# Performance work log

Hardware: AMD Instinct MI355X
Metric: run time of the kernel (lower is better)

Reference implementation:

```python
import jax, jax.numpy as jnp
import numpy as np

B, DIM, HID, K, G, MID = 1024, 384, 64, 8, 48, 128
EPS = 1e-06


def _gaussian_8x8():
    t = jnp.arange(K, dtype=jnp.float32) - 3.5
    g = jnp.exp(-(t[:, None] ** 2 + t[None, :] ** 2) / (2.0 * 2.0 ** 2))
    return g / g.sum()


def setup_inputs() -> dict:
    key = jax.random.key(0)
    ks = jax.random.split(key, 16)
    inp = {
        "x": jax.random.normal(ks[0], (B, DIM), dtype=jnp.float32),
        "W": jax.random.normal(ks[1], (DIM, HID), dtype=jnp.float32) * 0.02,
        "b": jax.random.normal(ks[2], (DIM, HID), dtype=jnp.float32) * 0.02,
        "patch_weight": _gaussian_8x8(),  # learnable 8x8, softmaxed in forward
        "pair_w1": jax.random.normal(ks[3], (G, G), dtype=jnp.float32) * 0.02,
        "pair_b1": jax.random.normal(ks[4], (G, G), dtype=jnp.float32) * 0.02,
        "pair_w2": jax.random.normal(ks[5], (G, G), dtype=jnp.float32) * 0.02,
        "pair_b2": jax.random.normal(ks[6], (G, G), dtype=jnp.float32) * 0.02,
        # nn.Linear(G, DIM)
        "proj_w": jax.random.normal(ks[7], (DIM, G), dtype=jnp.float32) * (1.0 / np.sqrt(G)),
        "proj_b": jax.random.normal(ks[8], (DIM,), dtype=jnp.float32) * 0.02,
        # nn.Linear(HID, MID)
        "down_w": jax.random.normal(ks[9], (MID, HID), dtype=jnp.float32) * (1.0 / np.sqrt(HID)),
        "down_b": jax.random.normal(ks[10], (MID,), dtype=jnp.float32) * 0.02,
        # nn.Linear(MID, HID)
        "up_w": jax.random.normal(ks[11], (HID, MID), dtype=jnp.float32) * (1.0 / np.sqrt(MID)),
        "up_b": jax.random.normal(ks[12], (HID,), dtype=jnp.float32) * 0.02,
    }
    return inp


def _leaky(v):
    return jnp.where(v >= 0, v, 0.01 * v)


def reference(x, W, b, patch_weight, pair_w1, pair_b1, pair_w2, pair_b2,
              proj_w, proj_b, down_w, down_b, up_w, up_b):
    # scale / inverse-bias GELU features: (B, DIM, HID)
    s = x[:, :, None]
    inv = 1.0 / (jnp.abs(s) + EPS)
    H = jax.nn.gelu(s * W[None] + inv * b[None], approximate=False)
    # Gram matrix over hidden dim: (B, DIM, DIM)
    P = jnp.einsum('bik,bjk->bij', H, H)
    # learnable gaussian patch pooling (softmax over flattened 8x8 weights)
    w = jax.nn.softmax(patch_weight.reshape(-1)).reshape(K, K)
    Pg = jnp.einsum('bgkhl,kl->bgh', P.reshape(-1, G, K, G, K), w)  # (B, G, G)
    # two elementwise gated leaky layers
    Pg = _leaky(Pg * pair_w1[None] + pair_b1[None])
    Pg = _leaky(Pg * pair_w2[None] + pair_b2[None])
    # softmax + nonlinear row reduction -> (B, G)
    row_soft = jax.nn.softmax(Pg, axis=-1)
    row_weights = (1.0 / (1.0 + row_soft ** 2)).sum(axis=-1)
    # project 48 -> 384, scale rows of H
    scales = row_weights @ proj_w.T + proj_b  # (B, DIM)
    H = H * scales[:, :, None]
    # tiny MLP on hidden dim
    z = _leaky(H @ down_w.T + down_b)
    z = _leaky(z @ up_w.T + up_b)
    return z
```

## Files before the change

kernel.cpp:

```cpp
#include <hip/hip_runtime.h>


#define EPSF 1e-6f

typedef __attribute__((ext_vector_type(8))) short bf16x8;
typedef __attribute__((ext_vector_type(4))) float f32x4;
typedef __attribute__((ext_vector_type(4))) unsigned short u16x4;

__device__ __forceinline__ unsigned short f2bf(float f) {
    union { float f; unsigned int u; } v; v.f = f;
    unsigned int r = v.u + 0x7fffu + ((v.u >> 16) & 1u);
    return (unsigned short)(r >> 16);
}
__device__ __forceinline__ float bf2f(unsigned short h) {
    union { unsigned int u; float f; } v; v.u = ((unsigned int)h) << 16;
    return v.f;
}
__device__ __forceinline__ float leaky(float v) { return fmaxf(v, 0.01f * v); }
__device__ __forceinline__ int key8(int r) { return (r ^ (r >> 3)) & 7; }
__device__ __forceinline__ float gelu_f(float u) {
    float t = u * (1.5957691216f + 0.0713548163f * (u * u));
    float e = __expf(t);
    float r = __builtin_amdgcn_rcpf(e + 1.0f);
    return fmaf(-u, r, u);
}

__global__ void prep(const float* __restrict__ proj_w,
                     const float* __restrict__ down_w,
                     const float* __restrict__ up_w,
                     float* __restrict__ ws) {
    int idx = blockIdx.x * blockDim.x + threadIdx.x;
    unsigned short* wb = (unsigned short*)(ws + 18432);
    if (idx < 18432) {
        int i = idx / 48, g = idx % 48;
        ws[g * 384 + i] = proj_w[idx];
    } else if (idx < 26624) {
        int k = idx - 18432;
        wb[k] = f2bf(down_w[k]);
    } else if (idx < 34816) {
        int k = idx - 26624;
        wb[8192 + k] = f2bf(up_w[k]);
    }
}

__global__ __launch_bounds__(1024, 4) void fused_main(
    const float* __restrict__ x,
    const float* __restrict__ W,
    const float* __restrict__ bb,
    const float* __restrict__ patch_weight,
    const float* __restrict__ pw1, const float* __restrict__ pb1,
    const float* __restrict__ pw2, const float* __restrict__ pb2,
    const float* __restrict__ proj_b,
    const float* __restrict__ down_b,
    const float* __restrict__ up_b,
    const float* __restrict__ ws,
    float* __restrict__ out)
{
    __shared__ __align__(16) unsigned short sH[24576];
    __shared__ __align__(16) unsigned short sRB[24576];
    __shared__ __align__(16) unsigned short sZ1[24576];
    __shared__ float sw[64];
    __shared__ float srw[48];
    __shared__ float sScale[384];
    __shared__ float sDb[128];
    __shared__ float sUb[64];

    const int t = threadIdx.x;
    const int b = blockIdx.x;
    const int wv = t >> 6, lane = t & 63, q = lane >> 4, r = lane & 15;
    const float* projT = ws;
    const unsigned short* dwB = (const unsigned short*)(ws + 18432);
    const unsigned short* uwB = dwB + 8192;
    unsigned short* sM  = sRB;
    unsigned short* sDW = sRB;
    unsigned short* sUW = sRB + 8192;
    float* sPg = (float*)(sRB + 16384);

    if (t < 64) {
        float p = patch_weight[t];
        float m = p;
        for (int o = 32; o > 0; o >>= 1) m = fmaxf(m, __shfl_xor(m, o));
        float e = __expf(p - m);
        float s = e;
        for (int o = 32; o > 0; o >>= 1) s += __shfl_xor(s, o);
        sw[t] = e * __builtin_amdgcn_rcpf(s);
    }

    for (int j = 0; j < 6; ++j) {
        int idx4 = j * 1024 + t;
        int base = idx4 * 4;
        int i = base >> 6, c0 = base & 63;
        float4 w4 = ((const float4*)W)[idx4];
        float4 b4 = ((const float4*)bb)[idx4];
        float xi  = x[b * 384 + i];
        float inv = __builtin_amdgcn_rcpf(fabsf(xi) + EPSF);
        u16x4 hv;
        hv[0] = f2bf(gelu_f(fmaf(xi, w4.x, inv * b4.x)));
        hv[1] = f2bf(gelu_f(fmaf(xi, w4.y, inv * b4.y)));
        hv[2] = f2bf(gelu_f(fmaf(xi, w4.z, inv * b4.z)));
        hv[3] = f2bf(gelu_f(fmaf(xi, w4.w, inv * b4.w)));
        int cb = c0 >> 3, cc = c0 & 7;
        *(u16x4*)&sH[i * 64 + ((cb ^ key8(i)) << 3) + cc] = hv;
    }
    __syncthreads();

    if (t < 768) {
        const int cb = t & 7, lq = (t >> 3) & 1, g = t >> 4;
        float acc[4][8];
        #pragma unroll
        for (int a = 0; a < 4; ++a)
            #pragma unroll
            for (int cc = 0; cc < 8; ++cc) acc[a][cc] = 0.0f;
        #pragma unroll
        for (int k = 0; k < 8; ++k) {
            int i = g * 8 + k;
            bf16x8 hv = *(const bf16x8*)&sH[i * 64 + ((cb ^ key8(i)) << 3)];
            f32x4 w4 = *(const f32x4*)&sw[k * 8 + lq * 4];
            float hf[8];
            #pragma unroll
            for (int cc = 0; cc < 8; ++cc) hf[cc] = bf2f((unsigned short)hv[cc]);
            #pragma unroll
            for (int a = 0; a < 4; ++a)
                #pragma unroll
                for (int cc = 0; cc < 8; ++cc) acc[a][cc] = fmaf(w4[a], hf[cc], acc[a][cc]);
        }
        #pragma unroll
        for (int a = 0; a < 4; ++a) {
            int l = lq * 4 + a;
            bf16x8 mv;
            #pragma unroll
            for (int cc = 0; cc < 8; ++cc) mv[cc] = (short)f2bf(acc[a][cc]);
            *(bf16x8*)&sM[g * 512 + ((l * 8 + (cb ^ key8(g))) << 3)] = mv;
        }
    }
    __syncthreads();

    f32x4 pacc = {0.f, 0.f, 0.f, 0.f};
    if (wv < 9) {
        const int tg = wv / 3, th = wv % 3;
        for (int ks = 0; ks < 16; ++ks) {
            int kf = ks * 32 + q * 8;
            int g = tg * 16 + r;
            int cbg = kf >> 3;
            int cbs = (cbg & ~7) | ((cbg ^ key8(g)) & 7);
            bf16x8 av = *(const bf16x8*)&sM[g * 512 + (cbs << 3)];
            int h = th * 16 + r;
            int i = h * 8 + (kf >> 6);
            int cbh = (kf & 63) >> 3;
            bf16x8 bv = *(const bf16x8*)&sH[i * 64 + ((cbh ^ key8(i)) << 3)];
            pacc = __builtin_amdgcn_mfma_f32_16x16x32_bf16(av, bv, pacc, 0, 0, 0);
        }
        #pragma unroll
        for (int reg = 0; reg < 4; ++reg) {
            int g = tg * 16 + q * 4 + reg;
            int h = th * 16 + r;
            int idx = g * 48 + h;
            float v = pacc[reg];
            v = leaky(fmaf(v, pw1[idx], pb1[idx]));
            v = leaky(fmaf(v, pw2[idx], pb2[idx]));
            pacc[reg] = v;
        }
    }
    __syncthreads();

    if (wv < 9) {
        const int tg = wv / 3, th = wv % 3;
        #pragma unroll
        for (int reg = 0; reg < 4; ++reg) {
            int g = tg * 16 + q * 4 + reg;
            int h = th * 16 + r;
            sPg[g * 49 + h] = pacc[reg];
        }
    } else {
        for (int cid = t - 576; cid < 2048; cid += 448) {
            if (cid < 1024) {
                int nrow = cid >> 3, cb = cid & 7;
                bf16x8 v = *(const bf16x8*)&dwB[cid * 8];
                *(bf16x8*)&sDW[nrow * 64 + ((cb ^ key8(nrow)) << 3)] = v;
            } else {
                int c2 = cid - 1024;
                int rrow = c2 >> 4, cb = c2 & 15;
                bf16x8 v = *(const bf16x8*)&uwB[c2 * 8];
                int cbs = (cb & 8) | ((cb ^ key8(rrow)) & 7);
                *(bf16x8*)&sUW[rrow * 128 + (cbs << 3)] = v;
            }
        }
    }
    if (t < 128) sDb[t] = down_b[t];
    else if (t < 192) sUb[t - 128] = up_b[t - 128];
    __syncthreads();

    {
        #pragma unroll
        for (int rr = 0; rr < 3; ++rr) {
            int row = wv + rr * 16;
            float v = (lane < 48) ? sPg[row * 49 + lane] : -1e30f;
            float m = v;
            for (int o = 32; o > 0; o >>= 1) m = fmaxf(m, __shfl_xor(m, o));
            float e = (lane < 48) ? __expf(v - m) : 0.0f;
            float s = e;
            for (int o = 32; o > 0; o >>= 1) s += __shfl_xor(s, o);
            float p = e * __builtin_amdgcn_rcpf(s);
            float rwv = (lane < 48) ? __builtin_amdgcn_rcpf(fmaf(p, p, 1.0f)) : 0.0f;
            for (int o = 32; o > 0; o >>= 1) rwv += __shfl_xor(rwv, o);
            if (lane == 0) srw[row] = rwv;
        }
    }
    __syncthreads();

    if (t < 384) {
        float s = proj_b[t];
        #pragma unroll 4
        for (int g = 0; g < 48; ++g) s = fmaf(srw[g], projT[g * 384 + t], s);
        sScale[t] = s;
    }
    __syncthreads();

    const int mg = wv >> 2, ng = wv & 3;
    for (int rt = 0; rt < 2; ++rt) {
        const int r0 = rt * 192;
        {
            f32x4 zacc[3][2];
            #pragma unroll
            for (int a = 0; a < 3; ++a)
                #pragma unroll
                for (int e = 0; e < 2; ++e) zacc[a][e] = (f32x4){0.f, 0.f, 0.f, 0.f};
            #pragma unroll
            for (int ks = 0; ks < 2; ++ks) {
                int cb = ks * 4 + q;
                bf16x8 af[3];
                #pragma unroll
                for (int a = 0; a < 3; ++a) {
                    int i = r0 + (mg * 3 + a) * 16 + r;
                    af[a] = *(const bf16x8*)&sH[i * 64 + ((cb ^ key8(i)) << 3)];
                }
                #pragma unroll
                for (int e = 0; e < 2; ++e) {
                    int n = (ng * 2 + e) * 16 + r;
                    bf16x8 bv = *(const bf16x8*)&sDW[n * 64 + ((cb ^ key8(n)) << 3)];
                    #pragma unroll
                    for (int a = 0; a < 3; ++a)
                        zacc[a][e] = __builtin_amdgcn_mfma_f32_16x16x32_bf16(af[a], bv, zacc[a][e], 0, 0, 0);
                }
            }
            #pragma unroll
            for (int a = 0; a < 3; ++a) {
                #pragma unroll
                for (int e = 0; e < 2; ++e) {
                    #pragma unroll
                    for (int reg = 0; reg < 4; ++reg) {
                        int rl = (mg * 3 + a) * 16 + q * 4 + reg;
                        int m = (ng * 2 + e) * 16 + r;
                        float v = leaky(fmaf(zacc[a][e][reg], sScale[r0 + rl], sDb[m]));
                        int cb2 = m >> 3;
                        int cbs2 = (cb2 & 8) | ((cb2 ^ key8(rl)) & 7);
                        sZ1[rl * 128 + (cbs2 << 3) + (m & 7)] = f2bf(v);
                    }
                }
            }
        }
        __syncthreads();
        {
            f32x4 oacc[3];
            #pragma unroll
            for (int a = 0; a < 3; ++a) oacc[a] = (f32x4){0.f, 0.f, 0.f, 0.f};
            #pragma unroll
            for (int ks = 0; ks < 4; ++ks) {
                int cb = ks * 4 + q;
                int cp = ng * 16 + r;
                int cbsB = (cb & 8) | ((cb ^ key8(cp)) & 7);
                bf16x8 bv = *(const bf16x8*)&sUW[cp * 128 + (cbsB << 3)];
                #pragma unroll
                for (int a = 0; a < 3; ++a) {
                    int rl = (mg * 3 + a) * 16 + r;
                    int cbsA = (cb & 8) | ((cb ^ key8(rl)) & 7);
                    bf16x8 av = *(const bf16x8*)&sZ1[rl * 128 + (cbsA << 3)];
                    oacc[a] = __builtin_amdgcn_mfma_f32_16x16x32_bf16(av, bv, oacc[a], 0, 0, 0);
                }
            }
            #pragma unroll
            for (int a = 0; a < 3; ++a) {
                #pragma unroll
                for (int reg = 0; reg < 4; ++reg) {
                    int i = r0 + (mg * 3 + a) * 16 + q * 4 + reg;
                    int cp = ng * 16 + r;
                    out[(b * 384 + i) * 64 + cp] = leaky(oacc[a][reg] + sUb[cp]);
                }
            }
        }
        __syncthreads();
    }
}

extern "C" void kernel_launch(void* const* d_in, const int* in_sizes, int n_in,
                              void* d_out, int out_size, void* d_ws, size_t ws_size,
                              hipStream_t stream) {
    const float* x      = (const float*)d_in[0];
    const float* W      = (const float*)d_in[1];
    const float* bb     = (const float*)d_in[2];
    const float* pw     = (const float*)d_in[3];
    const float* pw1    = (const float*)d_in[4];
    const float* pb1    = (const float*)d_in[5];
    const float* pw2    = (const float*)d_in[6];
    const float* pb2    = (const float*)d_in[7];
    const float* proj_w = (const float*)d_in[8];
    const float* proj_b = (const float*)d_in[9];
    const float* down_w = (const float*)d_in[10];
    const float* down_b = (const float*)d_in[11];
    const float* up_w   = (const float*)d_in[12];
    const float* up_b   = (const float*)d_in[13];
    float* out = (float*)d_out;
    float* ws  = (float*)d_ws;

    prep<<<(34816 + 255) / 256, 256, 0, stream>>>(proj_w, down_w, up_w, ws);
    fused_main<<<1024, 1024, 0, stream>>>(x, W, bb, pw, pw1, pb1, pw2, pb2,
                                          proj_b, down_b, up_b, ws, out);
}
```

Measured before the change: 197.6 us.

## Split fused kernel into scale kernel and MLP kernel with recomputed GELU

The single 1024-thread fused kernel becomes two kernels. The first computes H, the pooled Gram matrix and the per-row scales with 512 threads, doing the pooling and MFMA work in two rounds to halve the sM buffer, then writes the scales to workspace. The second runs 3072 smaller blocks that recompute H in registers for 128 rows each and apply the down/up MLP. This lowers shared memory per block and should raise occupancy and parallelism, at the cost of recomputing the GELU features, an extra launch and a global round trip for the scales.

```diff
diff --git a/kernel.cpp b/kernel.cpp
--- a/kernel.cpp
+++ b/kernel.cpp
@@ -21,9 +21,11 @@
 __device__ __forceinline__ float gelu_f(float u) {
     float t = u * (1.5957691216f + 0.0713548163f * (u * u));
     float e = __expf(t);
-    float r = __builtin_amdgcn_rcpf(e + 1.0f);
-    return fmaf(-u, r, u);
-}
+    float rc = __builtin_amdgcn_rcpf(e + 1.0f);
+    return fmaf(-u, rc, u);
+}
+
+#define SCALES_OFF 26624
 
 __global__ void prep(const float* __restrict__ proj_w,
                      const float* __restrict__ down_w,
@@ -43,7 +45,7 @@
     }
 }
 
-__global__ __launch_bounds__(1024, 4) void fused_main(
+__global__ __launch_bounds__(512, 4) void kernA(
     const float* __restrict__ x,
     const float* __restrict__ W,
     const float* __restrict__ bb,
@@ -51,30 +53,18 @@
     const float* __restrict__ pw1, const float* __restrict__ pb1,
     const float* __restrict__ pw2, const float* __restrict__ pb2,
     const float* __restrict__ proj_b,
-    const float* __restrict__ down_b,
-    const float* __restrict__ up_b,
     const float* __restrict__ ws,
-    float* __restrict__ out)
+    float* __restrict__ scales)
 {
     __shared__ __align__(16) unsigned short sH[24576];
-    __shared__ __align__(16) unsigned short sRB[24576];
-    __shared__ __align__(16) unsigned short sZ1[24576];
-    __shared__ float sw[64];
+    __shared__ __align__(16) unsigned short sM[12288];
+    __shared__ __align__(16) float sw[64];
     __shared__ float srw[48];
-    __shared__ float sScale[384];
-    __shared__ float sDb[128];
-    __shared__ float sUb[64];
-
-    const int t = threadIdx.x;
-    const int b = blockIdx.x;
+    float* sPg = (float*)sM;
+
+    const int t = threadIdx.x, b = blockIdx.x;
     const int wv = t >> 6, lane = t & 63, q = lane >> 4, r = lane & 15;
     const float* projT = ws;
-    const unsigned short* dwB = (const unsigned short*)(ws + 18432);
-    const unsigned short* uwB = dwB + 8192;
-    unsigned short* sM  = sRB;
-    unsigned short* sDW = sRB;
-    unsigned short* sUW = sRB + 8192;
-    float* sPg = (float*)(sRB + 16384);
 
     if (t < 64) {
         float p = patch_weight[t];
@@ -86,8 +76,8 @@
         sw[t] = e * __builtin_amdgcn_rcpf(s);
     }
 
-    for (int j = 0; j < 6; ++j) {
-        int idx4 = j * 1024 + t;
+    for (int j = 0; j < 12; ++j) {
+        int idx4 = j * 512 + t;
         int base = idx4 * 4;
         int i = base >> 6, c0 = base & 63;
         float4 w4 = ((const float4*)W)[idx4];
@@ -104,107 +94,92 @@
     }
     __syncthreads();
 
-    if (t < 768) {
-        const int cb = t & 7, lq = (t >> 3) & 1, g = t >> 4;
-        float acc[4][8];
-        #pragma unroll
-        for (int a = 0; a < 4; ++a)
-            #pragma unroll
-            for (int cc = 0; cc < 8; ++cc) acc[a][cc] = 0.0f;
-        #pragma unroll
-        for (int k = 0; k < 8; ++k) {
-            int i = g * 8 + k;
-            bf16x8 hv = *(const bf16x8*)&sH[i * 64 + ((cb ^ key8(i)) << 3)];
-            f32x4 w4 = *(const f32x4*)&sw[k * 8 + lq * 4];
-            float hf[8];
-            #pragma unroll
-            for (int cc = 0; cc < 8; ++cc) hf[cc] = bf2f((unsigned short)hv[cc]);
+    f32x4 pacc[2];
+    pacc[0] = (f32x4){0.f, 0.f, 0.f, 0.f};
+    pacc[1] = (f32x4){0.f, 0.f, 0.f, 0.f};
+    for (int rnd = 0; rnd < 2; ++rnd) {
+        if (t < 384) {
+            const int g = t >> 3, cb = t & 7;
+            float acc[4][8];
             #pragma unroll
             for (int a = 0; a < 4; ++a)
                 #pragma unroll
-                for (int cc = 0; cc < 8; ++cc) acc[a][cc] = fmaf(w4[a], hf[cc], acc[a][cc]);
-        }
-        #pragma unroll
-        for (int a = 0; a < 4; ++a) {
-            int l = lq * 4 + a;
-            bf16x8 mv;
+                for (int cc = 0; cc < 8; ++cc) acc[a][cc] = 0.0f;
             #pragma unroll
-            for (int cc = 0; cc < 8; ++cc) mv[cc] = (short)f2bf(acc[a][cc]);
-            *(bf16x8*)&sM[g * 512 + ((l * 8 + (cb ^ key8(g))) << 3)] = mv;
-        }
-    }
-    __syncthreads();
-
-    f32x4 pacc = {0.f, 0.f, 0.f, 0.f};
-    if (wv < 9) {
-        const int tg = wv / 3, th = wv % 3;
-        for (int ks = 0; ks < 16; ++ks) {
-            int kf = ks * 32 + q * 8;
-            int g = tg * 16 + r;
-            int cbg = kf >> 3;
-            int cbs = (cbg & ~7) | ((cbg ^ key8(g)) & 7);
-            bf16x8 av = *(const bf16x8*)&sM[g * 512 + (cbs << 3)];
-            int h = th * 16 + r;
-            int i = h * 8 + (kf >> 6);
-            int cbh = (kf & 63) >> 3;
-            bf16x8 bv = *(const bf16x8*)&sH[i * 64 + ((cbh ^ key8(i)) << 3)];
-            pacc = __builtin_amdgcn_mfma_f32_16x16x32_bf16(av, bv, pacc, 0, 0, 0);
-        }
+            for (int k = 0; k < 8; ++k) {
+                int i = g * 8 + k;
+                bf16x8 hv = *(const bf16x8*)&sH[i * 64 + ((cb ^ key8(i)) << 3)];
+                f32x4 w4 = *(const f32x4*)&sw[k * 8 + rnd * 4];
+                float hf[8];
+                #pragma unroll
+                for (int cc = 0; cc < 8; ++cc) hf[cc] = bf2f((unsigned short)hv[cc]);
+                #pragma unroll
+                for (int a = 0; a < 4; ++a)
+                    #pragma unroll
+                    for (int cc = 0; cc < 8; ++cc) acc[a][cc] = fmaf(w4[a], hf[cc], acc[a][cc]);
+            }
+            #pragma unroll
+            for (int a = 0; a < 4; ++a) {
+                int blk = a * 8 + cb;
+                int blkS = (blk & ~7) | ((blk ^ key8(g)) & 7);
+                bf16x8 mv;
+                #pragma unroll
+                for (int cc = 0; cc < 8; ++cc) mv[cc] = (short)f2bf(acc[a][cc]);
+                *(bf16x8*)&sM[g * 256 + (blkS << 3)] = mv;
+            }
+        }
+        __syncthreads();
+        #pragma unroll
+        for (int ti = 0; ti < 2; ++ti) {
+            if (ti == 1 && wv != 0) break;
+            int tt = (ti == 0) ? wv : 8;
+            int tg = tt / 3, th = tt % 3;
+            for (int ks = 0; ks < 8; ++ks) {
+                int kl = ks * 32 + q * 8;
+                int g = tg * 16 + r;
+                int blk = kl >> 3;
+                int blkS = (blk & ~7) | ((blk ^ key8(g)) & 7);
+                bf16x8 av = *(const bf16x8*)&sM[g * 256 + (blkS << 3)];
+                int kg = rnd * 256 + kl;
+                int i = (th * 16 + r) * 8 + (kg >> 6);
+                int c = kg & 63;
+                bf16x8 bv = *(const bf16x8*)&sH[i * 64 + (((c >> 3) ^ key8(i)) << 3)];
+                pacc[ti] = __builtin_amdgcn_mfma_f32_16x16x32_bf16(av, bv, pacc[ti], 0, 0, 0);
+            }
+        }
+        __syncthreads();
+    }
+
+    #pragma unroll
+    for (int ti = 0; ti < 2; ++ti) {
+        if (ti == 1 && wv != 0) break;
+        int tt = (ti == 0) ? wv : 8;
+        int tg = tt / 3, th = tt % 3;
         #pragma unroll
         for (int reg = 0; reg < 4; ++reg) {
             int g = tg * 16 + q * 4 + reg;
             int h = th * 16 + r;
             int idx = g * 48 + h;
-            float v = pacc[reg];
+            float v = pacc[ti][reg];
             v = leaky(fmaf(v, pw1[idx], pb1[idx]));
             v = leaky(fmaf(v, pw2[idx], pb2[idx]));
-            pacc[reg] = v;
-        }
-    }
-    __syncthreads();
-
-    if (wv < 9) {
-        const int tg = wv / 3, th = wv % 3;
-        #pragma unroll
-        for (int reg = 0; reg < 4; ++reg) {
-            int g = tg * 16 + q * 4 + reg;
-            int h = th * 16 + r;
-            sPg[g * 49 + h] = pacc[reg];
-        }
-    } else {
-        for (int cid = t - 576; cid < 2048; cid += 448) {
-            if (cid < 1024) {
-                int nrow = cid >> 3, cb = cid & 7;
-                bf16x8 v = *(const bf16x8*)&dwB[cid * 8];
-                *(bf16x8*)&sDW[nrow * 64 + ((cb ^ key8(nrow)) << 3)] = v;
-            } else {
-                int c2 = cid - 1024;
-                int rrow = c2 >> 4, cb = c2 & 15;
-                bf16x8 v = *(const bf16x8*)&uwB[c2 * 8];
-                int cbs = (cb & 8) | ((cb ^ key8(rrow)) & 7);
-                *(bf16x8*)&sUW[rrow * 128 + (cbs << 3)] = v;
-            }
-        }
-    }
-    if (t < 128) sDb[t] = down_b[t];
-    else if (t < 192) sUb[t - 128] = up_b[t - 128];
-    __syncthreads();
-
-    {
-        #pragma unroll
-        for (int rr = 0; rr < 3; ++rr) {
-            int row = wv + rr * 16;
-            float v = (lane < 48) ? sPg[row * 49 + lane] : -1e30f;
-            float m = v;
-            for (int o = 32; o > 0; o >>= 1) m = fmaxf(m, __shfl_xor(m, o));
-            float e = (lane < 48) ? __expf(v - m) : 0.0f;
-            float s = e;
-            for (int o = 32; o > 0; o >>= 1) s += __shfl_xor(s, o);
-            float p = e * __builtin_amdgcn_rcpf(s);
-            float rwv = (lane < 48) ? __builtin_amdgcn_rcpf(fmaf(p, p, 1.0f)) : 0.0f;
-            for (int o = 32; o > 0; o >>= 1) rwv += __shfl_xor(rwv, o);
-            if (lane == 0) srw[row] = rwv;
-        }
+            sPg[g * 48 + h] = v;
+        }
+    }
+    __syncthreads();
+
+    for (int rr = 0; rr < 6; ++rr) {
+        int row = wv * 6 + rr;
+        float v = (lane < 48) ? sPg[row * 48 + lane] : -1e30f;
+        float m = v;
+        for (int o = 32; o > 0; o >>= 1) m = fmaxf(m, __shfl_xor(m, o));
+        float e = (lane < 48) ? __expf(v - m) : 0.0f;
+        float s = e;
+        for (int o = 32; o > 0; o >>= 1) s += __shfl_xor(s, o);
+        float p = e * __builtin_amdgcn_rcpf(s);
+        float rwv = (lane < 48) ? __builtin_amdgcn_rcpf(fmaf(p, p, 1.0f)) : 0.0f;
+        for (int o = 32; o > 0; o >>= 1) rwv += __shfl_xor(rwv, o);
+        if (lane == 0) srw[row] = rwv;
     }
     __syncthreads();
 
@@ -212,83 +187,129 @@
         float s = proj_b[t];
         #pragma unroll 4
         for (int g = 0; g < 48; ++g) s = fmaf(srw[g], projT[g * 384 + t], s);
-        sScale[t] = s;
-    }
-    __syncthreads();
-
-    const int mg = wv >> 2, ng = wv & 3;
-    for (int rt = 0; rt < 2; ++rt) {
-        const int r0 = rt * 192;
-        {
-            f32x4 zacc[3][2];
-            #pragma unroll
-            for (int a = 0; a < 3; ++a)
-                #pragma unroll
-                for (int e = 0; e < 2; ++e) zacc[a][e] = (f32x4){0.f, 0.f, 0.f, 0.f};
-            #pragma unroll
-            for (int ks = 0; ks < 2; ++ks) {
-                int cb = ks * 4 + q;
-                bf16x8 af[3];
-                #pragma unroll
-                for (int a = 0; a < 3; ++a) {
-                    int i = r0 + (mg * 3 + a) * 16 + r;
-                    af[a] = *(const bf16x8*)&sH[i * 64 + ((cb ^ key8(i)) << 3)];
-                }
-                #pragma unroll
-                for (int e = 0; e < 2; ++e) {
-                    int n = (ng * 2 + e) * 16 + r;
-                    bf16x8 bv = *(const bf16x8*)&sDW[n * 64 + ((cb ^ key8(n)) << 3)];
-                    #pragma unroll
-                    for (int a = 0; a < 3; ++a)
-                        zacc[a][e] = __builtin_amdgcn_mfma_f32_16x16x32_bf16(af[a], bv, zacc[a][e], 0, 0, 0);
-                }
-            }
-            #pragma unroll
-            for (int a = 0; a < 3; ++a) {
-                #pragma unroll
-                for (int e = 0; e < 2; ++e) {
-                    #pragma unroll
-                    for (int reg = 0; reg < 4; ++reg) {
-                        int rl = (mg * 3 + a) * 16 + q * 4 + reg;
-                        int m = (ng * 2 + e) * 16 + r;
-                        float v = leaky(fmaf(zacc[a][e][reg], sScale[r0 + rl], sDb[m]));
-                        int cb2 = m >> 3;
-                        int cbs2 = (cb2 & 8) | ((cb2 ^ key8(rl)) & 7);
-                        sZ1[rl * 128 + (cbs2 << 3) + (m & 7)] = f2bf(v);
-                    }
-                }
-            }
-        }
-        __syncthreads();
-        {
-            f32x4 oacc[3];
-            #pragma unroll
-            for (int a = 0; a < 3; ++a) oacc[a] = (f32x4){0.f, 0.f, 0.f, 0.f};
-            #pragma unroll
-            for (int ks = 0; ks < 4; ++ks) {
-                int cb = ks * 4 + q;
-                int cp = ng * 16 + r;
-                int cbsB = (cb & 8) | ((cb ^ key8(cp)) & 7);
-                bf16x8 bv = *(const bf16x8*)&sUW[cp * 128 + (cbsB << 3)];
-                #pragma unroll
-                for (int a = 0; a < 3; ++a) {
-                    int rl = (mg * 3 + a) * 16 + r;
-                    int cbsA = (cb & 8) | ((cb ^ key8(rl)) & 7);
-                    bf16x8 av = *(const bf16x8*)&sZ1[rl * 128 + (cbsA << 3)];
-                    oacc[a] = __builtin_amdgcn_mfma_f32_16x16x32_bf16(av, bv, oacc[a], 0, 0, 0);
-                }
-            }
-            #pragma unroll
-            for (int a = 0; a < 3; ++a) {
-                #pragma unroll
-                for (int reg = 0; reg < 4; ++reg) {
-                    int i = r0 + (mg * 3 + a) * 16 + q * 4 + reg;
-                    int cp = ng * 16 + r;
-                    out[(b * 384 + i) * 64 + cp] = leaky(oacc[a][reg] + sUb[cp]);
-                }
-            }
-        }
-        __syncthreads();
+        scales[b * 384 + t] = s;
+    }
+}
+
+__global__ __launch_bounds__(512, 4) void kernB(
+    const float* __restrict__ x,
+    const float* __restrict__ W,
+    const float* __restrict__ bb,
+    const float* __restrict__ down_b,
+    const float* __restrict__ up_b,
+    const float* __restrict__ ws,
+    const float* __restrict__ scales,
+    float* __restrict__ out)
+{
+    __shared__ __align__(16) unsigned short sDW[8192];
+    __shared__ __align__(16) unsigned short sUW[8192];
+    __shared__ __align__(16) unsigned short sZ1[16384];
+    __shared__ float sSc[128], sXv[128], sIv[128], sDb[128], sUb[64];
+
+    const int t = threadIdx.x, blk = blockIdx.x;
+    const int wv = t >> 6, lane = t & 63, q = lane >> 4, r = lane & 15;
+    const int bIdx = blk / 3, roff = (blk % 3) * 128;
+    const unsigned short* dwB = (const unsigned short*)(ws + 18432);
+    const unsigned short* uwB = dwB + 8192;
+
+    if (t < 128) {
+        float xv = x[bIdx * 384 + roff + t];
+        sXv[t] = xv;
+        sIv[t] = __builtin_amdgcn_rcpf(fabsf(xv) + EPSF);
+        sSc[t] = scales[blk * 128 + t];
+        sDb[t] = down_b[t];
+    } else if (t < 192) {
+        sUb[t - 128] = up_b[t - 128];
+    }
+    for (int cid = t; cid < 2048; cid += 512) {
+        if (cid < 1024) {
+            int nrow = cid >> 3, cb = cid & 7;
+            bf16x8 v = *(const bf16x8*)&dwB[cid * 8];
+            *(bf16x8*)&sDW[nrow * 64 + ((cb ^ key8(nrow)) << 3)] = v;
+        } else {
+            int c2 = cid - 1024;
+            int rrow = c2 >> 4, cb = c2 & 15;
+            bf16x8 v = *(const bf16x8*)&uwB[c2 * 8];
+            int cbs = (cb & 8) | ((cb ^ key8(rrow)) & 7);
+            *(bf16x8*)&sUW[rrow * 128 + (cbs << 3)] = v;
+        }
+    }
+    __syncthreads();
+
+    const int iloc = wv * 16 + r;
+    bf16x8 afr[2];
+    {
+        float xv = sXv[iloc], iv = sIv[iloc];
+        const int i = roff + iloc;
+        #pragma unroll
+        for (int ks = 0; ks < 2; ++ks) {
+            const float4* Wp = (const float4*)&W[i * 64 + ks * 32 + q * 8];
+            const float4* Bp = (const float4*)&bb[i * 64 + ks * 32 + q * 8];
+            float4 wa = Wp[0], wc = Wp[1], ba = Bp[0], bc = Bp[1];
+            bf16x8 af;
+            af[0] = (short)f2bf(gelu_f(fmaf(xv, wa.x, iv * ba.x)));
+            af[1] = (short)f2bf(gelu_f(fmaf(xv, wa.y, iv * ba.y)));
+            af[2] = (short)f2bf(gelu_f(fmaf(xv, wa.z, iv * ba.z)));
+            af[3] = (short)f2bf(gelu_f(fmaf(xv, wa.w, iv * ba.w)));
+            af[4] = (short)f2bf(gelu_f(fmaf(xv, wc.x, iv * bc.x)));
+            af[5] = (short)f2bf(gelu_f(fmaf(xv, wc.y, iv * bc.y)));
+            af[6] = (short)f2bf(gelu_f(fmaf(xv, wc.z, iv * bc.z)));
+            af[7] = (short)f2bf(gelu_f(fmaf(xv, wc.w, iv * bc.w)));
+            afr[ks] = af;
+        }
+    }
+    f32x4 acc[8];
+    #pragma unroll
+    for (int nt = 0; nt < 8; ++nt) acc[nt] = (f32x4){0.f, 0.f, 0.f, 0.f};
+    #pragma unroll
+    for (int ks = 0; ks < 2; ++ks) {
+        int cb = ks * 4 + q;
+        #pragma unroll
+        for (int nt = 0; nt < 8; ++nt) {
+            int nrow = nt * 16 + r;
+            bf16x8 bv = *(const bf16x8*)&sDW[nrow * 64 + ((cb ^ key8(nrow)) << 3)];
+            acc[nt] = __builtin_amdgcn_mfma_f32_16x16x32_bf16(afr[ks], bv, acc[nt], 0, 0, 0);
+        }
+    }
+    #pragma unroll
+    for (int nt = 0; nt < 8; ++nt) {
+        #pragma unroll
+        for (int reg = 0; reg < 4; ++reg) {
+            int rl = wv * 16 + q * 4 + reg;
+            int m = nt * 16 + r;
+            float v = leaky(fmaf(acc[nt][reg], sSc[rl], sDb[m]));
+            int cb2 = m >> 3;
+            int cbs2 = (cb2 & 8) | ((cb2 ^ key8(rl)) & 7);
+            sZ1[rl * 128 + (cbs2 << 3) + (m & 7)] = f2bf(v);
+        }
+    }
+    __syncthreads();
+
+    f32x4 a2[4];
+    #pragma unroll
+    for (int nt = 0; nt < 4; ++nt) a2[nt] = (f32x4){0.f, 0.f, 0.f, 0.f};
+    #pragma unroll
+    for (int ks = 0; ks < 4; ++ks) {
+        int rl = wv * 16 + r;
+        int cb = ks * 4 + q;
+        int cbsA = (cb & 8) | ((cb ^ key8(rl)) & 7);
+        bf16x8 av = *(const bf16x8*)&sZ1[rl * 128 + (cbsA << 3)];
+        #pragma unroll
+        for (int nt = 0; nt < 4; ++nt) {
+            int cp = nt * 16 + r;
+            int cbsB = (cb & 8) | ((cb ^ key8(cp)) & 7);
+            bf16x8 bv = *(const bf16x8*)&sUW[cp * 128 + (cbsB << 3)];
+            a2[nt] = __builtin_amdgcn_mfma_f32_16x16x32_bf16(av, bv, a2[nt], 0, 0, 0);
+        }
+    }
+    #pragma unroll
+    for (int nt = 0; nt < 4; ++nt) {
+        #pragma unroll
+        for (int reg = 0; reg < 4; ++reg) {
+            int il = wv * 16 + q * 4 + reg;
+            int cp = nt * 16 + r;
+            out[(blk * 128 + il) * 64 + cp] = leaky(a2[nt][reg] + sUb[cp]);
+        }
     }
 }
 
@@ -311,8 +332,10 @@
     const float* up_b   = (const float*)d_in[13];
     float* out = (float*)d_out;
     float* ws  = (float*)d_ws;
+    float* scales = ws + SCALES_OFF;
 
     prep<<<(34816 + 255) / 256, 256, 0, stream>>>(proj_w, down_w, up_w, ws);
-    fused_main<<<1024, 1024, 0, stream>>>(x, W, bb, pw, pw1, pb1, pw2, pb2,
-                                          proj_b, down_b, up_b, ws, out);
-}
+    kernA<<<1024, 512, 0, stream>>>(x, W, bb, pw, pw1, pb1, pw2, pb2,
+                                    proj_b, ws, scales);
+    kernB<<<3072, 512, 0, stream>>>(x, W, bb, down_b, up_b, ws, scales, out);
+}
```

Result: slower. 228.3 us (+15.5%).
